# Kernel tuning notes

Measured on AMD Instinct MI355X. Metric: run time of the kernel, lower is better.

Reference implementation:

```python
import jax, jax.numpy as jnp
import numpy as np
import math

B, S, D, H, F, E, K, L, V = 1, 2048, 768, 12, 1536, 8, 2, 2, 32000


def _ln(x, w, b, eps=1e-5):
    m = x.mean(-1, keepdims=True)
    v = ((x - m) ** 2).mean(-1, keepdims=True)
    return (x - m) / jnp.sqrt(v + eps) * w + b


def setup_inputs() -> dict:
    key = jax.random.key(0)
    ks = jax.random.split(key, 16)
    std = 0.02
    inp = {
        'tokens': jax.random.randint(ks[0], (B, S), 0, V),
        'emb': jax.random.normal(ks[1], (V, D), jnp.float32) * std,
        'qkv_w': jax.random.normal(ks[2], (L, 3 * D, D), jnp.float32) * std,
        'qkv_b': jax.random.normal(ks[3], (L, 3 * D), jnp.float32) * std,
        'out_w': jax.random.normal(ks[4], (L, D, D), jnp.float32) * std,
        'out_b': jax.random.normal(ks[5], (L, D), jnp.float32) * std,
        'ln1_w': jnp.ones((L, D), jnp.float32),
        'ln1_b': jax.random.normal(ks[6], (L, D), jnp.float32) * std,
        'ln2_w': jnp.ones((L, D), jnp.float32),
        'ln2_b': jax.random.normal(ks[7], (L, D), jnp.float32) * std,
        'gate_w': jax.random.normal(ks[8], (L, E, D), jnp.float32) * std,
        'eg_w': jax.random.normal(ks[9], (L, E, F, D), jnp.float32) * std,
        'eu_w': jax.random.normal(ks[10], (L, E, F, D), jnp.float32) * std,
        'ed_w': jax.random.normal(ks[11], (L, E, D, F), jnp.float32) * std,
        'rms_w': jnp.ones((D,), jnp.float32),
    }
    return inp


def reference(tokens, emb, qkv_w, qkv_b, out_w, out_b, ln1_w, ln1_b,
              ln2_w, ln2_b, gate_w, eg_w, eu_w, ed_w, rms_w):
    Dh = D // H
    x = emb[tokens] * math.sqrt(D)  # (B,S,D)
    for l in range(L):
        # --- MultiheadAttention (batch_first, no mask, eval) ---
        qkv = x @ qkv_w[l].T + qkv_b[l]
        q, k, v = jnp.split(qkv, 3, axis=-1)
        q = q.reshape(B, S, H, Dh).transpose(0, 2, 1, 3)
        k = k.reshape(B, S, H, Dh).transpose(0, 2, 1, 3)
        v = v.reshape(B, S, H, Dh).transpose(0, 2, 1, 3)
        att = jax.nn.softmax(jnp.einsum('bhqd,bhkd->bhqk', q, k) / math.sqrt(Dh), axis=-1)
        o = jnp.einsum('bhqk,bhkd->bhqd', att, v).transpose(0, 2, 1, 3).reshape(B, S, D)
        o = o @ out_w[l].T + out_b[l]
        x = _ln(x + o, ln1_w[l], ln1_b[l])
        # --- SimpleDeepseekV3MoE: top-k gate, softmax over top-k scores ---
        gs = jnp.einsum('bsd,ed->bse', x, gate_w[l])
        topv, topi = jax.lax.top_k(gs, K)
        tw = jax.nn.softmax(topv, axis=-1)  # (B,S,K)
        # dense per-expert combine weight (0 for unselected experts)
        ew = jnp.sum(jax.nn.one_hot(topi, E, dtype=x.dtype) * tw[..., None], axis=-2)  # (B,S,E)
        hg = jax.nn.silu(jnp.einsum('bsd,efd->bsef', x, eg_w[l]))
        hu = jnp.einsum('bsd,efd->bsef', x, eu_w[l])
        ye = jnp.einsum('bsef,edf->bsed', hg * hu, ed_w[l])
        moe = jnp.einsum('bsed,bse->bsd', ye, ew)
        x = _ln(x + moe, ln2_w[l], ln2_b[l])
    # final RMSNorm (torch default eps=None -> finfo eps)
    rms = jnp.sqrt(jnp.mean(x * x, axis=-1, keepdims=True) + jnp.finfo(x.dtype).eps)
    x = x / rms * rms_w
    logits = x @ emb.T  # tied lm_head
    return logits
```

## Files before the change

kernel.cpp:

```cpp
#include <hip/hip_runtime.h>

#define SQ   2048
#define DM   768
#define NHD  12
#define DHD  64
#define FF   1536
#define NE   8
#define NL   2
#define NV   32000

typedef __attribute__((ext_vector_type(8))) short bf16x8;
typedef __attribute__((ext_vector_type(4))) float f32x4;

__device__ __forceinline__ unsigned short f2bf(float f) {
  unsigned u = __float_as_uint(f);
  return (unsigned short)((u + 0x7fffu + ((u >> 16) & 1u)) >> 16);
}
__device__ __forceinline__ float bf2f(unsigned short h) {
  return __uint_as_float(((unsigned)h) << 16);
}

#define GLD16(ldsp, gp) __builtin_amdgcn_global_load_lds( \
    (const __attribute__((address_space(1))) void*)(gp),  \
    (__attribute__((address_space(3))) void*)(ldsp), 16, 0, 0)

__global__ __launch_bounds__(256) void conv_k(const float* __restrict__ s,
    unsigned short* __restrict__ d) {
  size_t i = (size_t)(blockIdx.x * 256 + threadIdx.x) * 8;
  float4 a = *(const float4*)(s + i);
  float4 b = *(const float4*)(s + i + 4);
  int4 pk = make_int4(
      (int)((unsigned)f2bf(a.x) | ((unsigned)f2bf(a.y) << 16)),
      (int)((unsigned)f2bf(a.z) | ((unsigned)f2bf(a.w) << 16)),
      (int)((unsigned)f2bf(b.x) | ((unsigned)f2bf(b.y) << 16)),
      (int)((unsigned)f2bf(b.z) | ((unsigned)f2bf(b.w) << 16)));
  *(int4*)(d + i) = pk;
}

__global__ __launch_bounds__(256) void embed_k(const int* __restrict__ tok,
    const float* __restrict__ emb, float* __restrict__ x,
    unsigned short* __restrict__ xbf) {
  int idx = blockIdx.x * 256 + threadIdx.x;
  int s = idx / DM, d = idx % DM;
  float v = emb[(size_t)tok[s] * DM + d] * 27.712812921102035f;
  x[idx] = v;
  xbf[idx] = f2bf(v);
}

template<bool GATHER, bool BIAS, bool OBF16>
__global__ __launch_bounds__(256) void gemm_k(
    const unsigned short* __restrict__ A, long long lda, long long a_z,
    const unsigned short* __restrict__ B, long long ldb, long long b_z,
    const float* __restrict__ bias,
    void* __restrict__ C, long long ldc, long long c_z,
    int M, int N, int Kd, float scale,
    const int* __restrict__ glist, long long gl_z,
    const int* __restrict__ cnt, int mT, int nT, int Z)
{
  int nwg = gridDim.x, bid = blockIdx.x;
  int q = nwg >> 3, r = nwg & 7;
  int xcd = bid & 7, j = bid >> 3;
  int wid = (xcd < r ? xcd * (q + 1) : r * (q + 1) + (xcd - r) * q) + j;
  int z = wid % Z; int rem = wid / Z;
  int mt = rem % mT, nt = rem / mT;

  int Mz = cnt ? cnt[z] : M;
  int m0 = mt * 128, n0 = nt * 128;
  if (m0 >= Mz) return;

  const unsigned short* Ab = A + (size_t)z * a_z;
  const unsigned short* Bb = B + (size_t)z * b_z;

  __shared__ __align__(16) unsigned short As[128 * 64];
  __shared__ __align__(16) unsigned short Bs[128 * 64];

  int t = threadIdx.x, w = t >> 6, lane = t & 63;
  int wm = (w >> 1) * 64, wn = (w & 1) * 64;
  int fr = lane & 15, ksg = lane >> 4;
  int lrow = lane >> 3;
  int lchunk = ((lane & 7) ^ lrow) * 8;

  const unsigned short* ap[4];
  const unsigned short* bp[4];
  unsigned short* la[4];
  unsigned short* lb[4];
  #pragma unroll
  for (int i = 0; i < 4; ++i) {
    int rrow = w * 32 + i * 8 + lrow;
    int gr = m0 + rrow; if (gr >= Mz) gr = Mz - 1;
    int arow; if constexpr (GATHER) arow = glist[(size_t)z * gl_z + gr]; else arow = gr;
    ap[i] = Ab + (size_t)arow * lda + lchunk;
    int br = n0 + rrow; if (br >= N) br = N - 1;
    bp[i] = Bb + (size_t)br * ldb + lchunk;
    la[i] = &As[(w * 32 + i * 8) * 64];
    lb[i] = &Bs[(w * 32 + i * 8) * 64];
  }

  int rx = fr & 7;
  int off0 = ((0 + ksg) ^ rx) * 8;
  int off1 = ((4 + ksg) ^ rx) * 8;

  f32x4 acc[4][4] = {};

  for (int k0 = 0; k0 < Kd; k0 += 64) {
    #pragma unroll
    for (int i = 0; i < 4; ++i) GLD16(la[i], ap[i] + k0);
    #pragma unroll
    for (int i = 0; i < 4; ++i) GLD16(lb[i], bp[i] + k0);
    __syncthreads();
    #pragma unroll
    for (int kb = 0; kb < 2; ++kb) {
      int offk = kb ? off1 : off0;
      bf16x8 af[4], bv[4];
      #pragma unroll
      for (int m = 0; m < 4; ++m)
        af[m] = *(const bf16x8*)&As[(wm + m * 16 + fr) * 64 + offk];
      #pragma unroll
      for (int n = 0; n < 4; ++n)
        bv[n] = *(const bf16x8*)&Bs[(wn + n * 16 + fr) * 64 + offk];
      #pragma unroll
      for (int m = 0; m < 4; ++m)
        #pragma unroll
        for (int n = 0; n < 4; ++n)
          acc[m][n] = __builtin_amdgcn_mfma_f32_16x16x32_bf16(
              af[m], bv[n], acc[m][n], 0, 0, 0);
    }
    __syncthreads();
  }

  int rb = ksg * 4;
  #pragma unroll
  for (int m = 0; m < 4; ++m) {
    #pragma unroll
    for (int n = 0; n < 4; ++n) {
      int col = n0 + wn + n * 16 + fr;
      if (col >= N) continue;
      #pragma unroll
      for (int rr = 0; rr < 4; ++rr) {
        int row = m0 + wm + m * 16 + rb + rr;
        if (row >= Mz) continue;
        float v = acc[m][n][rr] * scale;
        if constexpr (BIAS) v += bias[col];
        size_t off = (size_t)z * c_z + (size_t)row * ldc + col;
        if constexpr (OBF16) ((unsigned short*)C)[off] = f2bf(v);
        else                 ((float*)C)[off] = v;
      }
    }
  }
}

__global__ __launch_bounds__(256) void transpose_v_k(
    const unsigned short* __restrict__ qkv, unsigned short* __restrict__ vt) {
  int kt = blockIdx.x;
  int h  = blockIdx.y;
  __shared__ unsigned short tile[64][72];
  int t = threadIdx.x;
  int r = t >> 2;
  int c0 = (t & 3) * 16;
  const unsigned short* src =
      qkv + (size_t)(kt * 64 + r) * (3 * DM) + 2 * DM + h * DHD + c0;
  *(int4*)&tile[r][c0]     = *(const int4*)(src);
  *(int4*)&tile[r][c0 + 8] = *(const int4*)(src + 8);
  __syncthreads();
  unsigned u[8];
  #pragma unroll
  for (int j = 0; j < 8; ++j)
    u[j] = (unsigned)tile[c0 + 2 * j][r] | ((unsigned)tile[c0 + 2 * j + 1][r] << 16);
  unsigned short* dst = vt + (size_t)(h * DHD + r) * SQ + kt * 64 + c0;
  *(int4*)dst       = make_int4((int)u[0], (int)u[1], (int)u[2], (int)u[3]);
  *(int4*)(dst + 8) = make_int4((int)u[4], (int)u[5], (int)u[6], (int)u[7]);
}

__global__ __launch_bounds__(256) void flash_k(
    const unsigned short* __restrict__ qkv,
    const unsigned short* __restrict__ vt,
    unsigned short* __restrict__ o)
{
  int nwg = gridDim.x, bid = blockIdx.x;
  int cpx = nwg >> 3;
  int wid = (bid & 7) * cpx + (bid >> 3);
  int h  = wid >> 5;
  int qt = wid & 31;
  int q0 = qt * 64;

  __shared__ __align__(16) unsigned short Ks[128 * 64];
  __shared__ __align__(16) unsigned short Vs[128 * 64];
  __shared__ __align__(16) unsigned short Ps[4][16 * 136];

  int t = threadIdx.x, w = t >> 6, lane = t & 63;
  int fr = lane & 15, ksg = lane >> 4;
  int lrow = lane >> 3;
  int lchunk = ((lane & 7) ^ lrow) * 8;

  const unsigned short* qbase = qkv + (size_t)q0 * (3 * DM) + h * DHD;
  #pragma unroll
  for (int i = 0; i < 2; ++i) {
    int rrow = w * 16 + i * 8 + lrow;
    GLD16(&Ks[(w * 16 + i * 8) * 64], qbase + (size_t)rrow * (3 * DM) + lchunk);
  }
  __syncthreads();
  bf16x8 qf[2];
  {
    int row = w * 16 + fr, ph = fr & 7;
    qf[0] = *(const bf16x8*)&Ks[row * 64 + ((ksg ^ ph) * 8)];
    qf[1] = *(const bf16x8*)&Ks[row * 64 + (((4 + ksg) ^ ph) * 8)];
  }
  __syncthreads();

  const unsigned short* kbase = qkv + DM + h * DHD;
  const unsigned short* vb = vt + (size_t)(h * DHD) * SQ;

  f32x4 oacc[4] = {};
  float m_r[4] = {-1e30f, -1e30f, -1e30f, -1e30f};
  float l_r[4] = {0.f, 0.f, 0.f, 0.f};

  for (int kt = 0; kt < SQ / 128; ++kt) {
    int kk0 = kt * 128;
    #pragma unroll
    for (int i = 0; i < 4; ++i) {
      int rrow = w * 32 + i * 8 + lrow;
      GLD16(&Ks[(w * 32 + i * 8) * 64],
            kbase + (size_t)(kk0 + rrow) * (3 * DM) + lchunk);
    }
    #pragma unroll
    for (int i = 0; i < 4; ++i) {
      int p = w * 32 + i * 8 + lrow;
      GLD16(&Vs[(w * 32 + i * 8) * 64],
            vb + (size_t)(p >> 1) * SQ + kk0 + (p & 1) * 64 + lchunk);
    }
    __syncthreads();

    f32x4 sacc[8] = {};
    #pragma unroll
    for (int kb = 0; kb < 2; ++kb) {
      #pragma unroll
      for (int n = 0; n < 8; ++n) {
        int row = n * 16 + fr;
        bf16x8 bvv = *(const bf16x8*)&Ks[row * 64 +
            (((kb * 4 + ksg) ^ (fr & 7)) * 8)];
        sacc[n] = __builtin_amdgcn_mfma_f32_16x16x32_bf16(
            qf[kb], bvv, sacc[n], 0, 0, 0);
      }
    }

    #pragma unroll
    for (int r = 0; r < 4; ++r) {
      float mx = sacc[0][r];
      #pragma unroll
      for (int n = 1; n < 8; ++n) mx = fmaxf(mx, sacc[n][r]);
      mx = fmaxf(mx, __shfl_xor(mx, 1));
      mx = fmaxf(mx, __shfl_xor(mx, 2));
      mx = fmaxf(mx, __shfl_xor(mx, 4));
      mx = fmaxf(mx, __shfl_xor(mx, 8));
      float mn = fmaxf(m_r[r], mx * 0.125f);
      float resc = __expf(m_r[r] - mn);
      m_r[r] = mn;
      #pragma unroll
      for (int n = 0; n < 4; ++n) oacc[n][r] *= resc;
      float rs = 0.f;
      #pragma unroll
      for (int n = 0; n < 8; ++n) {
        float p = __expf(sacc[n][r] * 0.125f - mn);
        rs += p;
        Ps[w][(ksg * 4 + r) * 136 + n * 16 + fr] = f2bf(p);
      }
      rs += __shfl_xor(rs, 1);
      rs += __shfl_xor(rs, 2);
      rs += __shfl_xor(rs, 4);
      rs += __shfl_xor(rs, 8);
      l_r[r] = l_r[r] * resc + rs;
    }

    #pragma unroll
    for (int ksi = 0; ksi < 4; ++ksi) {
      bf16x8 pa = *(const bf16x8*)&Ps[w][fr * 136 + ksi * 32 + ksg * 8];
      #pragma unroll
      for (int n = 0; n < 4; ++n) {
        int p = (n * 16 + fr) * 2 + (ksi >> 1);
        int c = (ksi & 1) * 4 + ksg;
        bf16x8 bvv = *(const bf16x8*)&Vs[p * 64 + ((c ^ (p & 7)) * 8)];
        oacc[n] = __builtin_amdgcn_mfma_f32_16x16x32_bf16(
            pa, bvv, oacc[n], 0, 0, 0);
      }
    }
    __syncthreads();
  }

  unsigned short* ob = o + (size_t)(q0 + w * 16) * DM + h * DHD;
  #pragma unroll
  for (int r = 0; r < 4; ++r) {
    float invl = 1.f / l_r[r];
    int qrow = ksg * 4 + r;
    #pragma unroll
    for (int n = 0; n < 4; ++n)
      ob[(size_t)qrow * DM + n * 16 + fr] = f2bf(oacc[n][r] * invl);
  }
}

__global__ __launch_bounds__(256) void add_ln_k(const float* __restrict__ xin,
    const float* __restrict__ add, const float* __restrict__ w,
    const float* __restrict__ b, float* __restrict__ xout,
    unsigned short* __restrict__ xbf) {
  int row = blockIdx.x, t = threadIdx.x;
  const float* xi = xin + (size_t)row * DM;
  const float* ai = add + (size_t)row * DM;
  float v[3]; float s = 0.f, sq = 0.f;
  #pragma unroll
  for (int i = 0; i < 3; ++i) {
    int idx = t + i * 256;
    v[i] = xi[idx] + ai[idx];
    s += v[i]; sq += v[i] * v[i];
  }
  #pragma unroll
  for (int o = 32; o; o >>= 1) { s += __shfl_xor(s, o); sq += __shfl_xor(sq, o); }
  __shared__ float rsm[4], rqm[4];
  int wv = t >> 6;
  if ((t & 63) == 0) { rsm[wv] = s; rqm[wv] = sq; }
  __syncthreads();
  s = rsm[0] + rsm[1] + rsm[2] + rsm[3];
  sq = rqm[0] + rqm[1] + rqm[2] + rqm[3];
  float mean = s * (1.f / 768.f);
  float var = sq * (1.f / 768.f) - mean * mean;
  float inv = rsqrtf(var + 1e-5f);
  float* xo = xout + (size_t)row * DM;
  unsigned short* xb = xbf + (size_t)row * DM;
  #pragma unroll
  for (int i = 0; i < 3; ++i) {
    int idx = t + i * 256;
    float y = (v[i] - mean) * inv * w[idx] + b[idx];
    xo[idx] = y; xb[idx] = f2bf(y);
  }
}

__global__ void gate_topk_k(const float* __restrict__ x, const float* __restrict__ gw,
    float* __restrict__ tw, int* __restrict__ ti, int* __restrict__ cnt,
    int* __restrict__ lists, int* __restrict__ slot) {
  int sIdx = blockIdx.x, lane = threadIdx.x;
  const float* xr = x + (size_t)sIdx * DM;
  float acc[NE] = {};
  for (int d = lane; d < DM; d += 64) {
    float xv = xr[d];
    #pragma unroll
    for (int e = 0; e < NE; ++e) acc[e] += xv * gw[e * DM + d];
  }
  #pragma unroll
  for (int e = 0; e < NE; ++e) {
    #pragma unroll
    for (int o = 32; o; o >>= 1) acc[e] += __shfl_down(acc[e], o);
  }
  if (lane == 0) {
    float v0 = -1e30f, v1 = -1e30f; int i0 = 0, i1 = 0;
    #pragma unroll
    for (int e = 0; e < NE; ++e) {
      float v = acc[e];
      if (v > v0) { v1 = v0; i1 = i0; v0 = v; i0 = e; }
      else if (v > v1) { v1 = v; i1 = e; }
    }
    float e1 = expf(v1 - v0);
    float inv = 1.f / (1.f + e1);
    tw[sIdx * 2] = inv; tw[sIdx * 2 + 1] = e1 * inv;
    ti[sIdx * 2] = i0;  ti[sIdx * 2 + 1] = i1;
    int p0 = atomicAdd(&cnt[i0], 1); lists[i0 * SQ + p0] = sIdx; slot[sIdx * 2] = p0;
    int p1 = atomicAdd(&cnt[i1], 1); lists[i1 * SQ + p1] = sIdx; slot[sIdx * 2 + 1] = p1;
  }
}

__global__ void zero_k(int* __restrict__ c) {
  if (threadIdx.x < NE) c[threadIdx.x] = 0;
}

__global__ __launch_bounds__(256) void silu_mul_k(unsigned short* __restrict__ hg,
    const unsigned short* __restrict__ hu, const int* __restrict__ cnt) {
  int e = blockIdx.y, sl = blockIdx.x;
  if (sl >= cnt[e]) return;
  size_t base = ((size_t)e * SQ + sl) * FF;
  int t = threadIdx.x;
  #pragma unroll
  for (int i = 0; i < FF / 256; ++i) {
    size_t idx = base + t + i * 256;
    float g = bf2f(hg[idx]);
    float u = bf2f(hu[idx]);
    float sv = g / (1.f + expf(-g));
    hg[idx] = f2bf(sv * u);
  }
}

__global__ __launch_bounds__(256) void combine_ln_k(const float* __restrict__ xin,
    const float* __restrict__ ye, const float* __restrict__ tw,
    const int* __restrict__ ti, const int* __restrict__ slot,
    const float* __restrict__ w, const float* __restrict__ b,
    float* __restrict__ xout, unsigned short* __restrict__ xbf) {
  int row = blockIdx.x, t = threadIdx.x;
  int e0 = ti[row * 2], e1 = ti[row * 2 + 1];
  int p0 = slot[row * 2], p1 = slot[row * 2 + 1];
  float w0 = tw[row * 2], w1 = tw[row * 2 + 1];
  const float* y0 = ye + ((size_t)e0 * SQ + p0) * DM;
  const float* y1 = ye + ((size_t)e1 * SQ + p1) * DM;
  const float* xi = xin + (size_t)row * DM;
  float v[3]; float s = 0.f, sq = 0.f;
  #pragma unroll
  for (int i = 0; i < 3; ++i) {
    int idx = t + i * 256;
    v[i] = xi[idx] + w0 * y0[idx] + w1 * y1[idx];
    s += v[i]; sq += v[i] * v[i];
  }
  #pragma unroll
  for (int o = 32; o; o >>= 1) { s += __shfl_xor(s, o); sq += __shfl_xor(sq, o); }
  __shared__ float rsm[4], rqm[4];
  int wv = t >> 6;
  if ((t & 63) == 0) { rsm[wv] = s; rqm[wv] = sq; }
  __syncthreads();
  s = rsm[0] + rsm[1] + rsm[2] + rsm[3];
  sq = rqm[0] + rqm[1] + rqm[2] + rqm[3];
  float mean = s * (1.f / 768.f);
  float var = sq * (1.f / 768.f) - mean * mean;
  float inv = rsqrtf(var + 1e-5f);
  float* xo = xout + (size_t)row * DM;
  unsigned short* xb = xbf + (size_t)row * DM;
  #pragma unroll
  for (int i = 0; i < 3; ++i) {
    int idx = t + i * 256;
    float y = (v[i] - mean) * inv * w[idx] + b[idx];
    xo[idx] = y; xb[idx] = f2bf(y);
  }
}

__global__ __launch_bounds__(256) void rms_k(const float* __restrict__ x,
    const float* __restrict__ rw, unsigned short* __restrict__ xbf) {
  int row = blockIdx.x, t = threadIdx.x;
  const float* xi = x + (size_t)row * DM;
  float v[3]; float sq = 0.f;
  #pragma unroll
  for (int i = 0; i < 3; ++i) {
    int idx = t + i * 256;
    v[i] = xi[idx];
    sq += v[i] * v[i];
  }
  #pragma unroll
  for (int o = 32; o; o >>= 1) sq += __shfl_xor(sq, o);
  __shared__ float rqm[4];
  int wv = t >> 6;
  if ((t & 63) == 0) rqm[wv] = sq;
  __syncthreads();
  sq = rqm[0] + rqm[1] + rqm[2] + rqm[3];
  float inv = rsqrtf(sq * (1.f / 768.f) + 1.1920929e-07f);
  unsigned short* xb = xbf + (size_t)row * DM;
  #pragma unroll
  for (int i = 0; i < 3; ++i) {
    int idx = t + i * 256;
    xb[idx] = f2bf(v[i] * inv * rw[idx]);
  }
}

extern "C" void kernel_launch(void* const* d_in, const int* in_sizes, int n_in,
                              void* d_out, int out_size, void* d_ws, size_t ws_size,
                              hipStream_t stream) {
  (void)in_sizes; (void)n_in; (void)out_size; (void)ws_size;
  const int*   tokens = (const int*)d_in[0];
  const float* emb    = (const float*)d_in[1];
  const float* qkv_w  = (const float*)d_in[2];
  const float* qkv_b  = (const float*)d_in[3];
  const float* out_w  = (const float*)d_in[4];
  const float* out_b  = (const float*)d_in[5];
  const float* ln1_w  = (const float*)d_in[6];
  const float* ln1_b  = (const float*)d_in[7];
  const float* ln2_w  = (const float*)d_in[8];
  const float* ln2_b  = (const float*)d_in[9];
  const float* gate_w = (const float*)d_in[10];
  const float* eg_w   = (const float*)d_in[11];
  const float* eu_w   = (const float*)d_in[12];
  const float* ed_w   = (const float*)d_in[13];
  const float* rms_w  = (const float*)d_in[14];
  float* out = (float*)d_out;

  char* wsb = (char*)d_ws;
  float*          x_f    = (float*)(wsb + 0);
  unsigned short* x_bf   = (unsigned short*)(wsb + 6291456);
  unsigned short* qkv_bf = (unsigned short*)(wsb + 9437184);
  unsigned short* vt     = (unsigned short*)(wsb + 18874368);
  unsigned short* o_bf   = (unsigned short*)(wsb + 22020096);
  float*          tmp_f  = (float*)(wsb + 25165824);
  float*          tw     = (float*)(wsb + 31457280);
  int*            ti     = (int*)(wsb + 31473664);
  int*            cnt    = (int*)(wsb + 31490048);
  int*            lists  = (int*)(wsb + 31490304);
  int*            slot   = (int*)(wsb + 31555840);
  unsigned short* emb_bf = (unsigned short*)(wsb + 31572224);
  unsigned short* wbf    = (unsigned short*)(wsb + 80724224);
  unsigned short* hg     = (unsigned short*)(wsb + 142065920);
  unsigned short* hu     = (unsigned short*)(wsb + 142065920 + 50331648);
  float*          ye     = (float*)(wsb + 142065920 + 50331648);

  unsigned short* qw_bf = wbf;
  unsigned short* ow_bf = wbf + 1769472;
  unsigned short* eg_bf = wbf + 2359296;
  unsigned short* eu_bf = wbf + 11796480;
  unsigned short* ed_bf = wbf + 21233664;

  conv_k<<<12000, 256, 0, stream>>>(emb, emb_bf);
  embed_k<<<SQ * DM / 256, 256, 0, stream>>>(tokens, emb, x_f, x_bf);

  for (int l = 0; l < NL; ++l) {
    const float* qw = qkv_w + (size_t)l * 3 * DM * DM;
    const float* qb = qkv_b + (size_t)l * 3 * DM;
    const float* ow = out_w + (size_t)l * DM * DM;
    const float* ob = out_b + (size_t)l * DM;
    const float* gw = gate_w + (size_t)l * NE * DM;
    const float* egw = eg_w + (size_t)l * NE * FF * DM;
    const float* euw = eu_w + (size_t)l * NE * FF * DM;
    const float* edw = ed_w + (size_t)l * NE * DM * FF;

    conv_k<<<864, 256, 0, stream>>>(qw, qw_bf);
    conv_k<<<288, 256, 0, stream>>>(ow, ow_bf);
    conv_k<<<4608, 256, 0, stream>>>(egw, eg_bf);
    conv_k<<<4608, 256, 0, stream>>>(euw, eu_bf);
    conv_k<<<4608, 256, 0, stream>>>(edw, ed_bf);

    gemm_k<false, true, true><<<16 * 18, 256, 0, stream>>>(
        x_bf, DM, 0, qw_bf, DM, 0, qb, qkv_bf, 3 * DM, 0,
        SQ, 3 * DM, DM, 1.f, nullptr, 0, nullptr, 16, 18, 1);

    transpose_v_k<<<dim3(SQ / 64, NHD), 256, 0, stream>>>(qkv_bf, vt);

    flash_k<<<NHD * 32, 256, 0, stream>>>(qkv_bf, vt, o_bf);

    gemm_k<false, true, false><<<16 * 6, 256, 0, stream>>>(
        o_bf, DM, 0, ow_bf, DM, 0, ob, tmp_f, DM, 0,
        SQ, DM, DM, 1.f, nullptr, 0, nullptr, 16, 6, 1);

    add_ln_k<<<SQ, 256, 0, stream>>>(x_f, tmp_f, ln1_w + l * DM, ln1_b + l * DM,
                                     x_f, x_bf);

    zero_k<<<1, 64, 0, stream>>>(cnt);
    gate_topk_k<<<SQ, 64, 0, stream>>>(x_f, gw, tw, ti, cnt, lists, slot);

    gemm_k<true, false, true><<<16 * 12 * NE, 256, 0, stream>>>(
        x_bf, DM, 0, eg_bf, DM, (long long)FF * DM, nullptr,
        hg, FF, (long long)SQ * FF,
        SQ, FF, DM, 1.f, lists, SQ, cnt, 16, 12, NE);
    gemm_k<true, false, true><<<16 * 12 * NE, 256, 0, stream>>>(
        x_bf, DM, 0, eu_bf, DM, (long long)FF * DM, nullptr,
        hu, FF, (long long)SQ * FF,
        SQ, FF, DM, 1.f, lists, SQ, cnt, 16, 12, NE);

    silu_mul_k<<<dim3(SQ, NE), 256, 0, stream>>>(hg, hu, cnt);

    gemm_k<false, false, false><<<16 * 6 * NE, 256, 0, stream>>>(
        hg, FF, (long long)SQ * FF, ed_bf, FF, (long long)DM * FF, nullptr,
        ye, DM, (long long)SQ * DM,
        SQ, DM, FF, 1.f, nullptr, 0, cnt, 16, 6, NE);

    combine_ln_k<<<SQ, 256, 0, stream>>>(x_f, ye, tw, ti, slot,
                                         ln2_w + l * DM, ln2_b + l * DM,
                                         x_f, x_bf);
  }

  rms_k<<<SQ, 256, 0, stream>>>(x_f, rms_w, x_bf);

  gemm_k<false, false, false><<<16 * 250, 256, 0, stream>>>(
      x_bf, DM, 0, emb_bf, DM, 0, nullptr, out, NV, 0,
      SQ, NV, DM, 1.f, nullptr, 0, nullptr, 16, 250, 1);
}
```

Baseline: 847.5 us.

## Add 128x256-tile triple-buffered GEMM kernel for the lm_head projection

Adds a dedicated 512-thread GEMM kernel with 128x256 output tiles, XOR-swizzled LDS layout, and a three-stage global_load_lds pipeline with prefetch split across the two k-halves. It replaces the generic gemm_k launch for the tied lm_head logits GEMM (2048x32000x768), halving the number of workgroups and doubling B-tile reuse per A load. The large LDS footprint (~144KB) limits occupancy to one block per CU and relies on hand-placed waitcnt/barrier ordering.

```diff
diff --git a/kernel.cpp b/kernel.cpp
--- a/kernel.cpp
+++ b/kernel.cpp
@@ -45,6 +45,130 @@
   float v = emb[(size_t)tok[s] * DM + d] * 27.712812921102035f;
   x[idx] = v;
   xbf[idx] = f2bf(v);
+}
+
+__global__ __launch_bounds__(512) void gemm256_k(
+    const unsigned short* __restrict__ A, long long lda,
+    const unsigned short* __restrict__ B, long long ldb,
+    float* __restrict__ C, long long ldc,
+    int Kd, int mT, int nT)
+{
+  int nwg = gridDim.x, bid = blockIdx.x;
+  int q = nwg >> 3, r = nwg & 7;
+  int xcd = bid & 7, j = bid >> 3;
+  int wid = (xcd < r ? xcd * (q + 1) : r * (q + 1) + (xcd - r) * q) + j;
+  int mt = wid % mT, nt = wid / mT;
+  int m0 = mt * 128, n0 = nt * 256;
+  (void)nT;
+
+  __shared__ __align__(16) unsigned short lds[3 * 6 * 4096];
+
+  int t = threadIdx.x, w = t >> 6, lane = t & 63;
+  int wm = (w >> 2) * 64, wn = (w & 3) * 64;
+  int fr = lane & 15, ksg = lane >> 4;
+  int lrow = lane >> 3;
+  int lchunk = ((lane & 7) ^ lrow) * 8;
+
+  const unsigned short* sp[6];
+  sp[0] = A + (size_t)(m0 +       w * 8 + lrow) * lda + lchunk;
+  sp[1] = A + (size_t)(m0 +  64 + w * 8 + lrow) * lda + lchunk;
+  #pragma unroll
+  for (int h = 0; h < 4; ++h)
+    sp[2 + h] = B + (size_t)(n0 + h * 64 + w * 8 + lrow) * ldb + lchunk;
+
+  int rdA = (w >> 2) * 4096;
+  int rdB = (2 + (w & 3)) * 4096;
+  int stDst = w * 512;
+
+  int rx = fr & 7;
+  int off0 = (ksg ^ rx) * 8;
+  int off1 = ((4 + ksg) ^ rx) * 8;
+
+  int KT = Kd >> 6;
+  f32x4 acc[4][4] = {};
+
+  #pragma unroll
+  for (int h = 0; h < 6; ++h)
+    GLD16(&lds[h * 4096 + stDst], sp[h]);
+  #pragma unroll
+  for (int h = 0; h < 6; ++h)
+    GLD16(&lds[(6 + h) * 4096 + stDst], sp[h] + 64);
+  asm volatile("s_waitcnt vmcnt(6)" ::: "memory");
+  __builtin_amdgcn_s_barrier();
+  __builtin_amdgcn_sched_barrier(0);
+
+  int buf = 0;
+  for (int kt = 0; kt < KT; ++kt) {
+    const unsigned short* Abl = &lds[buf * 6 * 4096 + rdA];
+    const unsigned short* Bbl = &lds[buf * 6 * 4096 + rdB];
+    int pf = (kt + 2 < KT);
+    int pbuf = buf + 2; if (pbuf >= 3) pbuf -= 3;
+    unsigned short* pd = &lds[pbuf * 6 * 4096 + stDst];
+    long long koff = (long long)(kt + 2) * 64;
+
+    if (pf) {
+      GLD16(pd + 0 * 4096, sp[0] + koff);
+      GLD16(pd + 1 * 4096, sp[1] + koff);
+      GLD16(pd + 2 * 4096, sp[2] + koff);
+    }
+    {
+      bf16x8 af[4], bv[4];
+      #pragma unroll
+      for (int m = 0; m < 4; ++m)
+        af[m] = *(const bf16x8*)&Abl[(m * 16 + fr) * 64 + off0];
+      #pragma unroll
+      for (int n = 0; n < 4; ++n)
+        bv[n] = *(const bf16x8*)&Bbl[(n * 16 + fr) * 64 + off0];
+      __builtin_amdgcn_s_setprio(1);
+      #pragma unroll
+      for (int m = 0; m < 4; ++m)
+        #pragma unroll
+        for (int n = 0; n < 4; ++n)
+          acc[m][n] = __builtin_amdgcn_mfma_f32_16x16x32_bf16(
+              af[m], bv[n], acc[m][n], 0, 0, 0);
+      __builtin_amdgcn_s_setprio(0);
+    }
+    if (pf) {
+      GLD16(pd + 3 * 4096, sp[3] + koff);
+      GLD16(pd + 4 * 4096, sp[4] + koff);
+      GLD16(pd + 5 * 4096, sp[5] + koff);
+    }
+    {
+      bf16x8 af[4], bv[4];
+      #pragma unroll
+      for (int m = 0; m < 4; ++m)
+        af[m] = *(const bf16x8*)&Abl[(m * 16 + fr) * 64 + off1];
+      #pragma unroll
+      for (int n = 0; n < 4; ++n)
+        bv[n] = *(const bf16x8*)&Bbl[(n * 16 + fr) * 64 + off1];
+      __builtin_amdgcn_s_setprio(1);
+      #pragma unroll
+      for (int m = 0; m < 4; ++m)
+        #pragma unroll
+        for (int n = 0; n < 4; ++n)
+          acc[m][n] = __builtin_amdgcn_mfma_f32_16x16x32_bf16(
+              af[m], bv[n], acc[m][n], 0, 0, 0);
+      __builtin_amdgcn_s_setprio(0);
+    }
+    if (pf) {
+      asm volatile("s_waitcnt vmcnt(6)" ::: "memory");
+    } else if (kt + 1 < KT) {
+      asm volatile("s_waitcnt vmcnt(0)" ::: "memory");
+    }
+    __builtin_amdgcn_s_barrier();
+    __builtin_amdgcn_sched_barrier(0);
+    buf = buf + 1; if (buf == 3) buf = 0;
+  }
+
+  int rb = ksg * 4;
+  #pragma unroll
+  for (int m = 0; m < 4; ++m)
+    #pragma unroll
+    for (int n = 0; n < 4; ++n)
+      #pragma unroll
+      for (int rr = 0; rr < 4; ++rr)
+        C[(size_t)(m0 + wm + m * 16 + rb + rr) * ldc + (n0 + wn + n * 16 + fr)] =
+            acc[m][n][rr];
 }
 
 template<bool GATHER, bool BIAS, bool OBF16>
@@ -557,7 +681,6 @@
 
   rms_k<<<SQ, 256, 0, stream>>>(x_f, rms_w, x_bf);
 
-  gemm_k<false, false, false><<<16 * 250, 256, 0, stream>>>(
-      x_bf, DM, 0, emb_bf, DM, 0, nullptr, out, NV, 0,
-      SQ, NV, DM, 1.f, nullptr, 0, nullptr, 16, 250, 1);
-}
+  gemm256_k<<<16 * 125, 512, 0, stream>>>(
+      x_bf, DM, emb_bf, DM, out, NV, DM, 16, 125);
+}
```

Measured after the change: 834.3 us. Within noise of the previous version (-1.6%).
